# Kernel tuning notes

Measured on AMD Instinct MI355X. Metric: run time of the kernel, lower is better.

Reference implementation:

```python
import jax, jax.numpy as jnp
import numpy as np

THRESH = 1.0
DECAY = 0.5


def setup_inputs() -> dict:
    key = jax.random.key(0)
    X = jax.random.normal(key, (32, 128, 32, 32, 16), dtype=jnp.float32)
    return {"X": X}


def reference(X):
    # Leaky-integrate-and-fire scan over the trailing time axis.
    Xt = jnp.moveaxis(X, -1, 0)  # [T, B, C, H, W] time-leading for scan

    def step(mem, x_t):
        mem = mem * DECAY + x_t                      # leaky integration
        s = (mem >= THRESH).astype(X.dtype)          # threshold spike
        mem = mem * (1.0 - s)                        # hard reset on spike
        return mem, s

    _, spikes = jax.lax.scan(step, jnp.zeros_like(Xt[0]), Xt)
    return jnp.moveaxis(spikes, 0, -1)  # back to [..., T]
```

## Files before the change

kernel.cpp:

```cpp
#include <hip/hip_runtime.h>


#define LIF_DECAY  0.5f
#define LIF_THRESH 1.0f

#define LIF_STEP(v)                                        \
    {                                                      \
        m = m * LIF_DECAY + (v);                           \
        float sp = (m >= LIF_THRESH) ? 1.0f : 0.0f;        \
        (v) = sp;                                          \
        m = (sp != 0.0f) ? 0.0f : m;                       \
    }

__global__ __launch_bounds__(256) void lif_kernel(const float4* __restrict__ X4,
                                                  float4* __restrict__ O4) {
    __shared__ float4 lds[4 * 257];

    const int tid = threadIdx.x;
    const size_t base = (size_t)blockIdx.x * 1024;

    const int q  = tid & 3;
    const int plc = (tid >> 2);

#pragma unroll
    for (int k = 0; k < 4; ++k) {
        float4 v = X4[base + (size_t)(k * 256 + tid)];
        lds[q * 257 + (k * 64 + plc)] = v;
    }
    __syncthreads();

    float4 f0 = lds[0 * 257 + tid];
    float4 f1 = lds[1 * 257 + tid];
    float4 f2 = lds[2 * 257 + tid];
    float4 f3 = lds[3 * 257 + tid];

    float m = 0.0f;
    LIF_STEP(f0.x) LIF_STEP(f0.y) LIF_STEP(f0.z) LIF_STEP(f0.w)
    LIF_STEP(f1.x) LIF_STEP(f1.y) LIF_STEP(f1.z) LIF_STEP(f1.w)
    LIF_STEP(f2.x) LIF_STEP(f2.y) LIF_STEP(f2.z) LIF_STEP(f2.w)
    LIF_STEP(f3.x) LIF_STEP(f3.y) LIF_STEP(f3.z) LIF_STEP(f3.w)

    __syncthreads();

    lds[0 * 257 + tid] = f0;
    lds[1 * 257 + tid] = f1;
    lds[2 * 257 + tid] = f2;
    lds[3 * 257 + tid] = f3;
    __syncthreads();

#pragma unroll
    for (int k = 0; k < 4; ++k) {
        O4[base + (size_t)(k * 256 + tid)] = lds[q * 257 + (k * 64 + plc)];
    }
}

extern "C" void kernel_launch(void* const* d_in, const int* in_sizes, int n_in,
                              void* d_out, int out_size, void* d_ws, size_t ws_size,
                              hipStream_t stream) {
    (void)n_in; (void)d_ws; (void)ws_size; (void)out_size;
    const float4* X4 = (const float4*)d_in[0];
    float4* O4 = (float4*)d_out;

    int n_f4 = in_sizes[0] / 4;
    int grid = n_f4 / 1024;
    lif_kernel<<<grid, 256, 0, stream>>>(X4, O4);
}
```

Before: 427.7 us.

## Process four tiles per block with register prefetch and nontemporal stores

```diff
diff --git a/kernel.cpp b/kernel.cpp
--- a/kernel.cpp
+++ b/kernel.cpp
@@ -3,6 +3,9 @@
 
 #define LIF_DECAY  0.5f
 #define LIF_THRESH 1.0f
+#define TILES_PER_BLOCK 4
+
+typedef float nfloat4 __attribute__((ext_vector_type(4)));
 
 #define LIF_STEP(v)                                        \
     {                                                      \
@@ -12,45 +15,65 @@
         m = (sp != 0.0f) ? 0.0f : m;                       \
     }
 
-__global__ __launch_bounds__(256) void lif_kernel(const float4* __restrict__ X4,
-                                                  float4* __restrict__ O4) {
-    __shared__ float4 lds[4 * 257];
+__global__ __launch_bounds__(256) void lif_kernel(const nfloat4* __restrict__ X4,
+                                                  nfloat4* __restrict__ O4) {
+    __shared__ nfloat4 lds[4 * 257];
 
     const int tid = threadIdx.x;
-    const size_t base = (size_t)blockIdx.x * 1024;
+    const int q   = tid & 3;
+    const int plc = tid >> 2;
 
-    const int q  = tid & 3;
-    const int plc = (tid >> 2);
+    size_t base = (size_t)blockIdx.x * (1024 * TILES_PER_BLOCK);
+
+    nfloat4 v0 = X4[base + (size_t)(0 * 256 + tid)];
+    nfloat4 v1 = X4[base + (size_t)(1 * 256 + tid)];
+    nfloat4 v2 = X4[base + (size_t)(2 * 256 + tid)];
+    nfloat4 v3 = X4[base + (size_t)(3 * 256 + tid)];
 
 #pragma unroll
-    for (int k = 0; k < 4; ++k) {
-        float4 v = X4[base + (size_t)(k * 256 + tid)];
-        lds[q * 257 + (k * 64 + plc)] = v;
-    }
-    __syncthreads();
+    for (int t = 0; t < TILES_PER_BLOCK; ++t) {
+        const size_t tbase = base + (size_t)t * 1024;
 
-    float4 f0 = lds[0 * 257 + tid];
-    float4 f1 = lds[1 * 257 + tid];
-    float4 f2 = lds[2 * 257 + tid];
-    float4 f3 = lds[3 * 257 + tid];
+        if (t > 0) __syncthreads();
 
-    float m = 0.0f;
-    LIF_STEP(f0.x) LIF_STEP(f0.y) LIF_STEP(f0.z) LIF_STEP(f0.w)
-    LIF_STEP(f1.x) LIF_STEP(f1.y) LIF_STEP(f1.z) LIF_STEP(f1.w)
-    LIF_STEP(f2.x) LIF_STEP(f2.y) LIF_STEP(f2.z) LIF_STEP(f2.w)
-    LIF_STEP(f3.x) LIF_STEP(f3.y) LIF_STEP(f3.z) LIF_STEP(f3.w)
+        lds[q * 257 + (0 * 64 + plc)] = v0;
+        lds[q * 257 + (1 * 64 + plc)] = v1;
+        lds[q * 257 + (2 * 64 + plc)] = v2;
+        lds[q * 257 + (3 * 64 + plc)] = v3;
+        __syncthreads();
 
-    __syncthreads();
+        nfloat4 f0 = lds[0 * 257 + tid];
+        nfloat4 f1 = lds[1 * 257 + tid];
+        nfloat4 f2 = lds[2 * 257 + tid];
+        nfloat4 f3 = lds[3 * 257 + tid];
 
-    lds[0 * 257 + tid] = f0;
-    lds[1 * 257 + tid] = f1;
-    lds[2 * 257 + tid] = f2;
-    lds[3 * 257 + tid] = f3;
-    __syncthreads();
+        if (t + 1 < TILES_PER_BLOCK) {
+            const size_t nbase = tbase + 1024;
+            v0 = X4[nbase + (size_t)(0 * 256 + tid)];
+            v1 = X4[nbase + (size_t)(1 * 256 + tid)];
+            v2 = X4[nbase + (size_t)(2 * 256 + tid)];
+            v3 = X4[nbase + (size_t)(3 * 256 + tid)];
+        }
+
+        float m = 0.0f;
+        LIF_STEP(f0.x) LIF_STEP(f0.y) LIF_STEP(f0.z) LIF_STEP(f0.w)
+        LIF_STEP(f1.x) LIF_STEP(f1.y) LIF_STEP(f1.z) LIF_STEP(f1.w)
+        LIF_STEP(f2.x) LIF_STEP(f2.y) LIF_STEP(f2.z) LIF_STEP(f2.w)
+        LIF_STEP(f3.x) LIF_STEP(f3.y) LIF_STEP(f3.z) LIF_STEP(f3.w)
+
+        __syncthreads();
+
+        lds[0 * 257 + tid] = f0;
+        lds[1 * 257 + tid] = f1;
+        lds[2 * 257 + tid] = f2;
+        lds[3 * 257 + tid] = f3;
+        __syncthreads();
 
 #pragma unroll
-    for (int k = 0; k < 4; ++k) {
-        O4[base + (size_t)(k * 256 + tid)] = lds[q * 257 + (k * 64 + plc)];
+        for (int k = 0; k < 4; ++k) {
+            nfloat4 s = lds[q * 257 + (k * 64 + plc)];
+            __builtin_nontemporal_store(s, &O4[tbase + (size_t)(k * 256 + tid)]);
+        }
     }
 }
 
@@ -58,10 +81,10 @@
                               void* d_out, int out_size, void* d_ws, size_t ws_size,
                               hipStream_t stream) {
     (void)n_in; (void)d_ws; (void)ws_size; (void)out_size;
-    const float4* X4 = (const float4*)d_in[0];
-    float4* O4 = (float4*)d_out;
+    const nfloat4* X4 = (const nfloat4*)d_in[0];
+    nfloat4* O4 = (nfloat4*)d_out;
 
     int n_f4 = in_sizes[0] / 4;
-    int grid = n_f4 / 1024;
+    int grid = n_f4 / (1024 * TILES_PER_BLOCK);
     lif_kernel<<<grid, 256, 0, stream>>>(X4, O4);
 }
```

Measured after the change: 450.6 us. 1.05x slower.

## Use per-wavefront LDS transpose without block barriers and nontemporal stores

Applied to the files above, without the earlier changes.

```diff
diff --git a/kernel.cpp b/kernel.cpp
--- a/kernel.cpp
+++ b/kernel.cpp
@@ -3,6 +3,9 @@
 
 #define LIF_DECAY  0.5f
 #define LIF_THRESH 1.0f
+#define PAD 65
+
+typedef float nfloat4 __attribute__((ext_vector_type(4)));
 
 #define LIF_STEP(v)                                        \
     {                                                      \
@@ -12,27 +15,33 @@
         m = (sp != 0.0f) ? 0.0f : m;                       \
     }
 
-__global__ __launch_bounds__(256) void lif_kernel(const float4* __restrict__ X4,
-                                                  float4* __restrict__ O4) {
-    __shared__ float4 lds[4 * 257];
+__global__ __launch_bounds__(256) void lif_kernel(const nfloat4* __restrict__ X4,
+                                                  nfloat4* __restrict__ O4) {
+    __shared__ nfloat4 lds[4][4 * PAD];
 
-    const int tid = threadIdx.x;
-    const size_t base = (size_t)blockIdx.x * 1024;
+    const int tid  = threadIdx.x;
+    const int lane = tid & 63;
+    const int wid  = tid >> 6;
 
-    const int q  = tid & 3;
-    const int plc = (tid >> 2);
+    const size_t wbase = ((size_t)blockIdx.x * 4 + wid) * 256;
+    nfloat4* __restrict__ L = &lds[wid][0];
 
-#pragma unroll
-    for (int k = 0; k < 4; ++k) {
-        float4 v = X4[base + (size_t)(k * 256 + tid)];
-        lds[q * 257 + (k * 64 + plc)] = v;
-    }
-    __syncthreads();
+    nfloat4 v0 = X4[wbase + (size_t)(0 * 64 + lane)];
+    nfloat4 v1 = X4[wbase + (size_t)(1 * 64 + lane)];
+    nfloat4 v2 = X4[wbase + (size_t)(2 * 64 + lane)];
+    nfloat4 v3 = X4[wbase + (size_t)(3 * 64 + lane)];
 
-    float4 f0 = lds[0 * 257 + tid];
-    float4 f1 = lds[1 * 257 + tid];
-    float4 f2 = lds[2 * 257 + tid];
-    float4 f3 = lds[3 * 257 + tid];
+    const int q  = lane & 3;
+    const int pl = lane >> 2;
+    L[q * PAD + (0 * 16 + pl)] = v0;
+    L[q * PAD + (1 * 16 + pl)] = v1;
+    L[q * PAD + (2 * 16 + pl)] = v2;
+    L[q * PAD + (3 * 16 + pl)] = v3;
+
+    nfloat4 f0 = L[0 * PAD + lane];
+    nfloat4 f1 = L[1 * PAD + lane];
+    nfloat4 f2 = L[2 * PAD + lane];
+    nfloat4 f3 = L[3 * PAD + lane];
 
     float m = 0.0f;
     LIF_STEP(f0.x) LIF_STEP(f0.y) LIF_STEP(f0.z) LIF_STEP(f0.w)
@@ -40,17 +49,15 @@
     LIF_STEP(f2.x) LIF_STEP(f2.y) LIF_STEP(f2.z) LIF_STEP(f2.w)
     LIF_STEP(f3.x) LIF_STEP(f3.y) LIF_STEP(f3.z) LIF_STEP(f3.w)
 
-    __syncthreads();
-
-    lds[0 * 257 + tid] = f0;
-    lds[1 * 257 + tid] = f1;
-    lds[2 * 257 + tid] = f2;
-    lds[3 * 257 + tid] = f3;
-    __syncthreads();
+    L[0 * PAD + lane] = f0;
+    L[1 * PAD + lane] = f1;
+    L[2 * PAD + lane] = f2;
+    L[3 * PAD + lane] = f3;
 
 #pragma unroll
     for (int k = 0; k < 4; ++k) {
-        O4[base + (size_t)(k * 256 + tid)] = lds[q * 257 + (k * 64 + plc)];
+        nfloat4 s = L[q * PAD + (k * 16 + pl)];
+        __builtin_nontemporal_store(s, &O4[wbase + (size_t)(k * 64 + lane)]);
     }
 }
 
@@ -58,8 +65,8 @@
                               void* d_out, int out_size, void* d_ws, size_t ws_size,
                               hipStream_t stream) {
     (void)n_in; (void)d_ws; (void)ws_size; (void)out_size;
-    const float4* X4 = (const float4*)d_in[0];
-    float4* O4 = (float4*)d_out;
+    const nfloat4* X4 = (const nfloat4*)d_in[0];
+    nfloat4* O4 = (nfloat4*)d_out;
 
     int n_f4 = in_sizes[0] / 4;
     int grid = n_f4 / 1024;
```

New measurement: 440.6 us. 3.0% more time.
